# Kernel optimization log

Hardware: AMD Instinct MI355X
Metric: run time of the kernel (lower is better)

Reference implementation:

```python
import math
import jax, jax.numpy as jnp
import numpy as np

NHID = 1024
HEADS = 16
SEQ = 1024
BATCH = 8


def setup_inputs() -> dict:
    key = jax.random.key(0)
    ks = jax.random.split(key, 12)
    s = 0.02
    inp = {
        "query": jax.random.normal(ks[0], (SEQ, BATCH, NHID), jnp.float32),
        "key": jax.random.normal(ks[1], (SEQ, BATCH, NHID), jnp.float32),
        "value": jax.random.normal(ks[2], (SEQ, BATCH, NHID), jnp.float32),
        "qs_p": jax.random.normal(ks[3], (1, 1, NHID), jnp.float32) * s,
        "ks_p": jax.random.normal(ks[4], (1, 1, NHID), jnp.float32) * s,
        "vs_p": jax.random.normal(ks[5], (1, 1, NHID), jnp.float32) * s,
        "Wq": jax.random.normal(ks[6], (NHID, NHID), jnp.float32) * s,
        "bq": jax.random.normal(ks[7], (NHID,), jnp.float32) * s,
        "Wzf": jax.random.normal(ks[8], (2 * NHID, NHID), jnp.float32) * s,
        "bzf": jax.random.normal(ks[9], (2 * NHID,), jnp.float32) * s,
    }
    # additive causal mask, viewed as (1,1,S,S) and added to scores
    causal = jnp.triu(jnp.ones((SEQ, SEQ), jnp.float32), k=1) * (-1e9)
    inp["attn_mask"] = causal
    return inp


def reference(query, key, value, qs_p, ks_p, vs_p, Wq, bq, Wzf, bzf, attn_mask):
    nhid = NHID
    heads = HEADS
    dim = nhid // heads

    # sigmoid gates on Q/K/V scales
    qs = jax.nn.sigmoid(qs_p)              # (1,1,nhid)
    ks_g = jax.nn.sigmoid(ks_p)
    vs_in = jax.nn.sigmoid(vs_p)

    # QRNNLayer(window=1, output_gate=False) on single-step vs:
    # z = tanh(Wz vs + bz), f = sigmoid(Wf vs + bf), h = f * z (h0 = 0)
    zf = jnp.einsum('abn,mn->abm', vs_in, Wzf) + bzf   # (1,1,2*nhid)
    z = jnp.tanh(zf[..., :nhid])
    f = jax.nn.sigmoid(zf[..., nhid:])
    vs = f * z                                          # (1,1,nhid)

    # q projection (k,v have no Linear with defaults)
    q_lin = jnp.einsum('sbn,mn->sbm', query, Wq) + bq

    q = qs * q_lin       # (S,B,nhid)
    k = ks_g * key
    v = vs * value

    # seq-first -> batch-first, split heads
    def split_heads(t):
        t = t.transpose(1, 0, 2)                         # (B,S,nhid)
        B, S, _ = t.shape
        return t.reshape(B, S, heads, dim).transpose(0, 2, 1, 3)  # (B,H,S,d)

    qh, kh, vh = split_heads(q), split_heads(k), split_heads(v)

    scores = jnp.einsum('bhqd,bhkd->bhqk', qh, kh) / math.sqrt(dim)
    scores = scores + attn_mask[None, None]              # (B,H,S,S)
    weights = jax.nn.softmax(scores, axis=-1)
    mix = jnp.einsum('bhqk,bhkd->bhqd', weights, vh)     # (B,H,S,d)

    B = mix.shape[0]
    mix = mix.transpose(0, 2, 1, 3).reshape(B, -1, nhid)  # (B,S,nhid)
    mix = mix.transpose(1, 0, 2)                          # (S,B,nhid) seq-first
    return mix, weights
```

## Files before the change

### kernel.cpp

```cpp
#include <hip/hip_runtime.h>

typedef unsigned short u16;
typedef unsigned int   u32;
typedef float  f32x4  __attribute__((ext_vector_type(4)));
typedef short  bf16x8 __attribute__((ext_vector_type(8)));
typedef unsigned short u16x8 __attribute__((ext_vector_type(8)));
typedef unsigned short u16x4 __attribute__((ext_vector_type(4)));
typedef unsigned int   u32x2 __attribute__((ext_vector_type(2)));

#define DEV __device__ __forceinline__

constexpr int S  = 1024;
constexpr int BB = 8;
constexpr int NH = 1024;
constexpr int H  = 16;

DEV u16 f2bf(float f) {
  union { float f; unsigned u; } v{f};
  unsigned r = v.u + 0x7FFFu + ((v.u >> 16) & 1u);
  return (u16)(r >> 16);
}
DEV float sigm(float x) { return 1.0f / (1.0f + __expf(-x)); }
DEV float exp2a(float x) { float r; asm("v_exp_f32 %0, %1" : "=v"(r) : "v"(x)); return r; }

DEV void gload_lds16(const void* g, void* l) {
  __builtin_amdgcn_global_load_lds(
      (const __attribute__((address_space(1))) unsigned int*)g,
      (__attribute__((address_space(3))) unsigned int*)l, 16, 0, 0);
}

DEV f32x4 ntload4(const float* p) {
  return __builtin_nontemporal_load((const f32x4*)p);
}
DEV void ntstore4(f32x4 v, float* p) {
  __builtin_nontemporal_store(v, (f32x4*)p);
}

constexpr float SC = 0.18033688f;

__global__ __launch_bounds__(256) void k_prep(
    const float* __restrict__ query, const float* __restrict__ key,
    const float* __restrict__ value, const float* __restrict__ qs_p,
    const float* __restrict__ ks_p,  const float* __restrict__ vs_p,
    const float* __restrict__ Wq,   const float* __restrict__ bq,
    const float* __restrict__ Wzf,  const float* __restrict__ bzf,
    u16* __restrict__ qx, u16* __restrict__ kout, u16* __restrict__ vout,
    float* __restrict__ vsg, float* __restrict__ bq2, u16* __restrict__ wq_bf)
{
  __shared__ float tile[64][65];
  if (blockIdx.x >= 4096) {
    int m = (blockIdx.x - 4096) * 4 + (threadIdx.x >> 6);
    int l = threadIdx.x & 63;
    const float* wz = Wzf + (size_t)m * NH;
    const float* wf = Wzf + (size_t)(m + NH) * NH;
    int base = l * 16;
    float za = 0.f, fa = 0.f;
#pragma unroll
    for (int i = 0; i < 16; i += 4) {
      f32x4 vp  = *(const f32x4*)(vs_p + base + i);
      f32x4 wzv = *(const f32x4*)(wz + base + i);
      f32x4 wfv = *(const f32x4*)(wf + base + i);
      float v0 = sigm(vp.x), v1 = sigm(vp.y), v2 = sigm(vp.z), v3 = sigm(vp.w);
      za += v0 * wzv.x + v1 * wzv.y + v2 * wzv.z + v3 * wzv.w;
      fa += v0 * wfv.x + v1 * wfv.y + v2 * wfv.z + v3 * wfv.w;
    }
#pragma unroll
    for (int off = 1; off < 64; off <<= 1) {
      za += __shfl_xor(za, off);
      fa += __shfl_xor(fa, off);
    }
    float z   = tanhf(za + bzf[m]);
    float f   = sigm(fa + bzf[m + NH]);
    float qsm = sigm(qs_p[m]);
    if (l == 0) {
      vsg[m] = f * z;
      bq2[m] = qsm * bq[m] * SC;
    }
    float qss = qsm * SC;
    const float* wqr = Wq + (size_t)m * NH;
    u16* dst = wq_bf + (size_t)m * NH + base;
#pragma unroll
    for (int i = 0; i < 16; i += 4) {
      f32x4 wv = *(const f32x4*)(wqr + base + i);
      u16x4 o;
      o[0] = f2bf(qss * wv.x); o[1] = f2bf(qss * wv.y);
      o[2] = f2bf(qss * wv.z); o[3] = f2bf(qss * wv.w);
      *(u16x4*)(dst + i) = o;
    }
    return;
  }
  size_t idx = ((size_t)blockIdx.x * 256 + threadIdx.x) * 8;
  {
    f32x4 a = ntload4(query + idx);
    f32x4 b = ntload4(query + idx + 4);
    u16x8 o;
    o[0] = f2bf(a.x); o[1] = f2bf(a.y); o[2] = f2bf(a.z); o[3] = f2bf(a.w);
    o[4] = f2bf(b.x); o[5] = f2bf(b.y); o[6] = f2bf(b.z); o[7] = f2bf(b.w);
    *(u16x8*)(qx + idx) = o;
  }
  {
    int n0 = (int)(idx & 1023);
    int b  = (int)((idx >> 10) & 7);
    int s  = (int)(idx >> 13);
    f32x4 a  = ntload4(key + idx);
    f32x4 c  = ntload4(key + idx + 4);
    f32x4 k0 = *(const f32x4*)(ks_p + n0);
    f32x4 k1 = *(const f32x4*)(ks_p + n0 + 4);
    int h = n0 >> 6, d0 = n0 & 63;
    u16* dst = kout + (((size_t)(b * H + h) * S + s) * 64 + d0);
    u16x8 o;
    o[0] = f2bf(a.x * sigm(k0.x)); o[1] = f2bf(a.y * sigm(k0.y));
    o[2] = f2bf(a.z * sigm(k0.z)); o[3] = f2bf(a.w * sigm(k0.w));
    o[4] = f2bf(c.x * sigm(k1.x)); o[5] = f2bf(c.y * sigm(k1.y));
    o[6] = f2bf(c.z * sigm(k1.z)); o[7] = f2bf(c.w * sigm(k1.w));
    *(u16x8*)dst = o;
  }
  if (blockIdx.x < 2048) {
    int bh = blockIdx.x >> 4, kt = blockIdx.x & 15;
    int b = bh >> 4, h = bh & 15;
    int t = threadIdx.x;
    int sp = t >> 2, c0 = (t & 3) * 16;
    const float* src = value + ((size_t)(kt * 64 + sp) * (BB * NH) + b * NH + h * 64 + c0);
#pragma unroll
    for (int i = 0; i < 16; i += 4) {
      f32x4 v = ntload4(src + i);
      tile[sp][c0 + i + 0] = v.x;
      tile[sp][c0 + i + 1] = v.y;
      tile[sp][c0 + i + 2] = v.z;
      tile[sp][c0 + i + 3] = v.w;
    }
    __syncthreads();
    int d = t >> 2, s0 = (t & 3) * 16;
    u16* dst = vout + (((size_t)bh * 16 + kt) * 64 + d) * 64 + s0;
    u16x8 o0, o1;
#pragma unroll
    for (int i = 0; i < 8; ++i) o0[i] = f2bf(tile[s0 + i][d]);
#pragma unroll
    for (int i = 0; i < 8; ++i) o1[i] = f2bf(tile[s0 + 8 + i][d]);
    *(u16x8*)dst       = o0;
    *(u16x8*)(dst + 8) = o1;
  }
}

__global__ __launch_bounds__(512, 4) void k_attn(
    const u16* __restrict__ qx, const u16* __restrict__ wqb,
    const float* __restrict__ bq2, const u16* __restrict__ kws,
    const u16* __restrict__ vtw, const float* __restrict__ vsg,
    float* __restrict__ mix, float* __restrict__ wout)
{
  __shared__ __align__(16) char smem[65536];
  int bid = blockIdx.x;
  int b = bid & 7;
  int idx = bid >> 3;
  int h = idx & 15, t = 7 - (idx >> 4);
  int bh = b * 16 + h;
  int tid = threadIdx.x, w = tid >> 6, l = tid & 63;
  int g = l >> 4, lq = l & 15;
  int q0 = t * 128;
  int myq = q0 + 16 * w + lq;
  int jmax = 2 * t + 1;
  int jd = 2 * t + (w >> 2);
  float* wbase = wout + (size_t)bh * S * S;
  int srow = l >> 3, sblk = l & 7;

  u16* As = (u16*)smem;
  u16* Bs = (u16*)(smem + 32768);
  u16* Qs = (u16*)smem;
  u16* KVf = (u16*)(smem + 16384);
  u16* K2  = (u16*)smem;
  u16* V2  = (u16*)(smem + 24576);

  {
    size_t qrowbase = (size_t)(q0 * 8 + b) * 1024;
    auto stageA = [&](int kt, int buf) {
#pragma unroll
      for (int ii = 0; ii < 2; ++ii) {
        int i = w * 2 + ii;
        int row = i * 8 + srow;
        int blk = sblk ^ (row & 7);
        gload_lds16(qx + qrowbase + (size_t)row * 8192 + kt * 64 + blk * 8,
                    &As[buf * 8192 + i * 512]);
      }
    };
    auto stageB = [&](int kt, int buf) {
      int row = w * 8 + srow;
      int blk = sblk ^ (row & 7);
      gload_lds16(wqb + (size_t)(h * 64 + row) * 1024 + kt * 64 + blk * 8,
                  &Bs[buf * 4096 + w * 512]);
    };
    f32x4 acc[4];
    f32x4 zero4 = {0.f, 0.f, 0.f, 0.f};
#pragma unroll
    for (int fj = 0; fj < 4; ++fj) acc[fj] = zero4;
    stageA(0, 0); stageB(0, 0);
    for (int kt = 0; kt < 16; ++kt) {
      asm volatile("s_waitcnt vmcnt(0)" ::: "memory");
      __builtin_amdgcn_sched_barrier(0);
      __builtin_amdgcn_s_barrier();
      __builtin_amdgcn_sched_barrier(0);
      if (kt < 15) { stageA(kt + 1, (kt + 1) & 1); stageB(kt + 1, (kt + 1) & 1); }
      __builtin_amdgcn_sched_barrier(0);
      int ab = (kt & 1) * 8192, bb = (kt & 1) * 4096;
      __builtin_amdgcn_s_setprio(1);
#pragma unroll
      for (int kk = 0; kk < 2; ++kk) {
        int ar = 16 * w + lq;
        bf16x8 av = *(const bf16x8*)&As[ab + ar * 64 + ((((kk << 2) + g) ^ (ar & 7)) << 3)];
#pragma unroll
        for (int fj = 0; fj < 4; ++fj) {
          int br = fj * 16 + lq;
          bf16x8 bv = *(const bf16x8*)&Bs[bb + br * 64 + ((((kk << 2) + g) ^ (br & 7)) << 3)];
          acc[fj] = __builtin_amdgcn_mfma_f32_16x16x32_bf16(av, bv, acc[fj], 0, 0, 0);
        }
      }
      __builtin_amdgcn_s_setprio(0);
    }
    float bq4[4];
#pragma unroll
    for (int fj = 0; fj < 4; ++fj) bq4[fj] = bq2[h * 64 + fj * 16 + lq];
#pragma unroll
    for (int fj = 0; fj < 4; ++fj) {
      int d = fj * 16 + lq;
#pragma unroll
      for (int r = 0; r < 4; ++r) {
        int qrow = 16 * w + (g << 2) + r;
        Qs[qrow * 64 + (((fj * 2 + (d >> 3 & 1)) ^ (qrow & 7)) << 3) + (d & 7)] =
            f2bf(acc[fj][r] + bq4[fj]);
      }
    }
    __syncthreads();
  }
  bf16x8 qa[2];
#pragma unroll
  for (int kk = 0; kk < 2; ++kk) {
    int qr = 16 * w + lq;
    qa[kk] = *(const bf16x8*)&Qs[qr * 64 + ((((kk << 2) + g) ^ (qr & 7)) << 3)];
  }
  asm volatile("s_waitcnt lgkmcnt(0)" ::: "memory");
  __builtin_amdgcn_sched_barrier(0);
  __builtin_amdgcn_s_barrier();

  auto stageK1 = [&](int j, int buf) {
    int row = w * 8 + srow;
    int blk = sblk ^ (row & 7);
    gload_lds16(kws + ((size_t)bh * S + j * 64 + row) * 64 + blk * 8,
                &KVf[buf * 4096 + w * 512]);
  };

  stageK1(0, 0);
  if (jmax >= 1) stageK1(1, 1);
  if (jmax >= 2) stageK1(2, 2);
  float lsum = 0.f;
  for (int j = 0; j <= jmax; ++j) {
    if (j + 2 <= jmax)      asm volatile("s_waitcnt vmcnt(2)" ::: "memory");
    else if (j + 1 <= jmax) asm volatile("s_waitcnt vmcnt(1)" ::: "memory");
    else                    asm volatile("s_waitcnt vmcnt(0)" ::: "memory");
    __builtin_amdgcn_sched_barrier(0);
    __builtin_amdgcn_s_barrier();
    __builtin_amdgcn_sched_barrier(0);
    if (j + 3 <= jmax) stageK1(j + 3, (j + 3) & 3);
    __builtin_amdgcn_sched_barrier(0);
    if (j <= jd) {
      int jb = (j & 3) * 4096;
      f32x4 sacc[4];
      f32x4 zero4 = {0.f, 0.f, 0.f, 0.f};
#pragma unroll
      for (int fj = 0; fj < 4; ++fj) sacc[fj] = zero4;
      __builtin_amdgcn_s_setprio(1);
#pragma unroll
      for (int kk = 0; kk < 2; ++kk)
#pragma unroll
        for (int fj = 0; fj < 4; ++fj) {
          int kr = fj * 16 + lq;
          bf16x8 kb = *(const bf16x8*)&KVf[jb + kr * 64 + ((((kk << 2) + g) ^ (kr & 7)) << 3)];
          sacc[fj] = __builtin_amdgcn_mfma_f32_16x16x32_bf16(kb, qa[kk], sacc[fj], 0, 0, 0);
        }
      __builtin_amdgcn_s_setprio(0);
      if (j < jd) {
#pragma unroll
        for (int fj = 0; fj < 4; ++fj)
#pragma unroll
          for (int r = 0; r < 4; ++r) lsum += exp2a(sacc[fj][r]);
      } else {
#pragma unroll
        for (int fj = 0; fj < 4; ++fj)
#pragma unroll
          for (int r = 0; r < 4; ++r) {
            int ki = j * 64 + fj * 16 + 4 * g + r;
            if (ki <= myq) lsum += exp2a(sacc[fj][r]);
          }
      }
    }
  }
  lsum += __shfl_xor(lsum, 16);
  lsum += __shfl_xor(lsum, 32);
  float invl = 1.0f / lsum;

  __builtin_amdgcn_s_barrier();

  auto stageK2 = [&](int j, int buf) {
    int row = w * 8 + srow;
    int blk = sblk ^ (row & 7);
    gload_lds16(kws + ((size_t)bh * S + j * 64 + row) * 64 + blk * 8,
                smem + buf * 8192 + w * 1024);
  };
  auto stageV2 = [&](int j, int buf) {
    int row = w * 8 + srow;
    int blk = sblk ^ (row & 7);
    gload_lds16(vtw + (((size_t)bh * 16 + j) * 64 + row) * 64 + blk * 8,
                smem + 24576 + buf * 8192 + w * 1024);
  };
  stageK2(0, 0); stageV2(0, 0);
  stageK2(1, 1); stageV2(1, 1);
  int bcur = 0;
  f32x4 oacc[4];
  {
    f32x4 zero4 = {0.f, 0.f, 0.f, 0.f};
#pragma unroll
    for (int db = 0; db < 4; ++db) oacc[db] = zero4;
  }
  char* pb = smem + 49152 + w * 2048;
  int pswz = (lq & 7) * 16;
  for (int j = 0; j <= jmax; ++j) {
    if (j == 0)            asm volatile("s_waitcnt vmcnt(2)" ::: "memory");
    else if (j == 1) {
      if (jmax >= 2)       asm volatile("s_waitcnt vmcnt(6)" ::: "memory");
      else                 asm volatile("s_waitcnt vmcnt(4)" ::: "memory");
    }
    else if (j < jmax)     asm volatile("s_waitcnt vmcnt(10)" ::: "memory");
    else                   asm volatile("s_waitcnt vmcnt(8)" ::: "memory");
    __builtin_amdgcn_sched_barrier(0);
    __builtin_amdgcn_s_barrier();
    __builtin_amdgcn_sched_barrier(0);
    if (j + 2 <= jmax) {
      int tb = bcur + 2; if (tb >= 3) tb -= 3;
      stageK2(j + 2, tb); stageV2(j + 2, tb);
    }
    __builtin_amdgcn_sched_barrier(0);
    if (j > jd) {
      f32x4 z4 = {0.f, 0.f, 0.f, 0.f};
#pragma unroll
      for (int fj = 0; fj < 4; ++fj)
        ntstore4(z4, wbase + (size_t)myq * S + j * 64 + fj * 16 + g * 4);
    } else {
      int kbase = bcur * 4096;
      f32x4 sacc[4];
      f32x4 zero4 = {0.f, 0.f, 0.f, 0.f};
#pragma unroll
      for (int fj = 0; fj < 4; ++fj) sacc[fj] = zero4;
      __builtin_amdgcn_s_setprio(1);
#pragma unroll
      for (int kk = 0; kk < 2; ++kk)
#pragma unroll
        for (int fj = 0; fj < 4; ++fj) {
          int kr = fj * 16 + lq;
          bf16x8 kb = *(const bf16x8*)&K2[kbase + kr * 64 + ((((kk << 2) + g) ^ (kr & 7)) << 3)];
          sacc[fj] = __builtin_amdgcn_mfma_f32_16x16x32_bf16(kb, qa[kk], sacc[fj], 0, 0, 0);
        }
      __builtin_amdgcn_s_setprio(0);
      bool diag = (j == jd);
      float p0[4], p1[4], p2[4], p3[4];
#pragma unroll
      for (int fj = 0; fj < 4; ++fj) {
        float* pp = fj == 0 ? p0 : fj == 1 ? p1 : fj == 2 ? p2 : p3;
#pragma unroll
        for (int r = 0; r < 4; ++r) {
          float e = exp2a(sacc[fj][r]) * invl;
          if (diag) {
            int ki = j * 64 + fj * 16 + 4 * g + r;
            if (ki > myq) e = 0.f;
          }
          pp[r] = e;
        }
      }
#pragma unroll
      for (int fj = 0; fj < 4; ++fj) {
        float* pp = fj == 0 ? p0 : fj == 1 ? p1 : fj == 2 ? p2 : p3;
        u32 w0, w1;
        asm("v_cvt_pk_bf16_f32 %0, %1, %2" : "=v"(w0) : "v"(pp[0]), "v"(pp[1]));
        asm("v_cvt_pk_bf16_f32 %0, %1, %2" : "=v"(w1) : "v"(pp[2]), "v"(pp[3]));
        u32x2 wv = {w0, w1};
        *(u32x2*)(pb + lq * 128 + ((fj * 32 + g * 8) ^ pswz)) = wv;
      }
#pragma unroll
      for (int fj = 0; fj < 4; ++fj) {
        float* pp = fj == 0 ? p0 : fj == 1 ? p1 : fj == 2 ? p2 : p3;
        f32x4 f4 = {pp[0], pp[1], pp[2], pp[3]};
        ntstore4(f4, wbase + (size_t)myq * S + j * 64 + fj * 16 + g * 4);
      }
      asm volatile("s_waitcnt lgkmcnt(0)" ::: "memory");
      __builtin_amdgcn_sched_barrier(0);
      __builtin_amdgcn_s_setprio(1);
#pragma unroll
      for (int kk = 0; kk < 2; ++kk) {
        bf16x8 pa = *(const bf16x8*)(pb + lq * 128 + ((kk * 64 + g * 16) ^ pswz));
#pragma unroll
        for (int db = 0; db < 4; ++db) {
          int d = db * 16 + lq;
          bf16x8 vb = *(const bf16x8*)&V2[bcur * 4096 + d * 64 + ((((kk << 2) + g) ^ (d & 7)) << 3)];
          oacc[db] = __builtin_amdgcn_mfma_f32_16x16x32_bf16(pa, vb, oacc[db], 0, 0, 0);
        }
      }
      __builtin_amdgcn_s_setprio(0);
    }
    bcur = (bcur == 2) ? 0 : bcur + 1;
  }

  float vs4[4];
#pragma unroll
  for (int db = 0; db < 4; ++db) vs4[db] = vsg[h * 64 + db * 16 + lq];
#pragma unroll
  for (int db = 0; db < 4; ++db) {
#pragma unroll
    for (int r = 0; r < 4; ++r) {
      int qi = q0 + 16 * w + 4 * g + r;
      __builtin_nontemporal_store(oacc[db][r] * vs4[db],
          mix + (size_t)(qi * BB + b) * NH + h * 64 + db * 16 + lq);
    }
  }

  {
    f32x4 z4 = {0.f, 0.f, 0.f, 0.f};
    int cstart = (jmax + 1) * 64;
    for (int lr = 0; lr < 16; ++lr) {
      float* rowp = wbase + (size_t)(q0 + 16 * w + lr) * S;
      for (int c = cstart + l * 4; c < S; c += 256)
        ntstore4(z4, rowp + c);
    }
  }
}

extern "C" void kernel_launch(void* const* d_in, const int* in_sizes, int n_in,
                              void* d_out, int out_size, void* d_ws, size_t ws_size,
                              hipStream_t stream) {
  (void)in_sizes; (void)n_in; (void)out_size; (void)ws_size;
  const float* query = (const float*)d_in[0];
  const float* key   = (const float*)d_in[1];
  const float* value = (const float*)d_in[2];
  const float* qs_p  = (const float*)d_in[3];
  const float* ks_p  = (const float*)d_in[4];
  const float* vs_p  = (const float*)d_in[5];
  const float* Wq    = (const float*)d_in[6];
  const float* bq    = (const float*)d_in[7];
  const float* Wzf   = (const float*)d_in[8];
  const float* bzf   = (const float*)d_in[9];

  char* ws = (char*)d_ws;
  float* vsg  = (float*)(ws + 0x1000);
  float* bq2  = (float*)(ws + 0x2000);
  u16* wq_bf  = (u16*)(ws + 0x4000);
  u16* qx_bf  = (u16*)(ws + 0x204000);
  u16* k_ws   = (u16*)(ws + 0x1204000);
  u16* vt_ws  = (u16*)(ws + 0x2204000);

  float* mix  = (float*)d_out;
  float* wout = mix + (size_t)S * BB * NH;

  k_prep<<<4352, 256, 0, stream>>>(query, key, value, qs_p, ks_p, vs_p,
                                   Wq, bq, Wzf, bzf,
                                   qx_bf, k_ws, vt_ws, vsg, bq2, wq_bf);
  k_attn<<<1024, 512, 0, stream>>>(qx_bf, wq_bf, bq2, k_ws, vt_ws, vsg,
                                   mix, wout);
}
```

Baseline: 224.1 us.

## Halve attention query tile to 64 rows with 256-thread blocks

```diff
diff --git a/kernel.cpp b/kernel.cpp
--- a/kernel.cpp
+++ b/kernel.cpp
@@ -142,51 +142,51 @@
   }
 }
 
-__global__ __launch_bounds__(512, 4) void k_attn(
+__global__ __launch_bounds__(256, 4) void k_attn(
     const u16* __restrict__ qx, const u16* __restrict__ wqb,
     const float* __restrict__ bq2, const u16* __restrict__ kws,
     const u16* __restrict__ vtw, const float* __restrict__ vsg,
     float* __restrict__ mix, float* __restrict__ wout)
 {
-  __shared__ __align__(16) char smem[65536];
+  __shared__ __align__(16) char smem[40960];
   int bid = blockIdx.x;
   int b = bid & 7;
   int idx = bid >> 3;
-  int h = idx & 15, t = 7 - (idx >> 4);
+  int h = idx & 15, t = 15 - (idx >> 4);
   int bh = b * 16 + h;
   int tid = threadIdx.x, w = tid >> 6, l = tid & 63;
   int g = l >> 4, lq = l & 15;
-  int q0 = t * 128;
+  int q0 = t * 64;
   int myq = q0 + 16 * w + lq;
-  int jmax = 2 * t + 1;
-  int jd = 2 * t + (w >> 2);
+  int jmax = t;
   float* wbase = wout + (size_t)bh * S * S;
   int srow = l >> 3, sblk = l & 7;
 
   u16* As = (u16*)smem;
-  u16* Bs = (u16*)(smem + 32768);
+  u16* Bs = (u16*)(smem + 16384);
   u16* Qs = (u16*)smem;
-  u16* KVf = (u16*)(smem + 16384);
-  u16* K2  = (u16*)smem;
-  u16* V2  = (u16*)(smem + 24576);
+  u16* K1 = (u16*)(smem + 8192);
+  u16* K2 = (u16*)(smem + 8192);
+  u16* V2 = (u16*)(smem + 24576);
 
   {
-    size_t qrowbase = (size_t)(q0 * 8 + b) * 1024;
     auto stageA = [&](int kt, int buf) {
 #pragma unroll
       for (int ii = 0; ii < 2; ++ii) {
-        int i = w * 2 + ii;
-        int row = i * 8 + srow;
+        int row = w * 16 + ii * 8 + srow;
         int blk = sblk ^ (row & 7);
-        gload_lds16(qx + qrowbase + (size_t)row * 8192 + kt * 64 + blk * 8,
-                    &As[buf * 8192 + i * 512]);
+        gload_lds16(qx + ((size_t)((q0 + row) * 8 + b) * 1024 + kt * 64 + blk * 8),
+                    &As[buf * 4096 + (w * 2 + ii) * 512]);
       }
     };
     auto stageB = [&](int kt, int buf) {
-      int row = w * 8 + srow;
-      int blk = sblk ^ (row & 7);
-      gload_lds16(wqb + (size_t)(h * 64 + row) * 1024 + kt * 64 + blk * 8,
-                  &Bs[buf * 4096 + w * 512]);
+#pragma unroll
+      for (int ii = 0; ii < 2; ++ii) {
+        int row = w * 16 + ii * 8 + srow;
+        int blk = sblk ^ (row & 7);
+        gload_lds16(wqb + ((size_t)(h * 64 + row) * 1024 + kt * 64 + blk * 8),
+                    &Bs[buf * 4096 + (w * 2 + ii) * 512]);
+      }
     };
     f32x4 acc[4];
     f32x4 zero4 = {0.f, 0.f, 0.f, 0.f};
@@ -200,7 +200,7 @@
       __builtin_amdgcn_sched_barrier(0);
       if (kt < 15) { stageA(kt + 1, (kt + 1) & 1); stageB(kt + 1, (kt + 1) & 1); }
       __builtin_amdgcn_sched_barrier(0);
-      int ab = (kt & 1) * 8192, bb = (kt & 1) * 4096;
+      int ab = (kt & 1) * 4096, bb = (kt & 1) * 4096;
       __builtin_amdgcn_s_setprio(1);
 #pragma unroll
       for (int kk = 0; kk < 2; ++kk) {
@@ -241,55 +241,55 @@
   __builtin_amdgcn_s_barrier();
 
   auto stageK1 = [&](int j, int buf) {
-    int row = w * 8 + srow;
-    int blk = sblk ^ (row & 7);
-    gload_lds16(kws + ((size_t)bh * S + j * 64 + row) * 64 + blk * 8,
-                &KVf[buf * 4096 + w * 512]);
+#pragma unroll
+    for (int ii = 0; ii < 2; ++ii) {
+      int row = w * 16 + ii * 8 + srow;
+      int blk = sblk ^ (row & 7);
+      gload_lds16(kws + ((size_t)bh * S + j * 64 + row) * 64 + blk * 8,
+                  &K1[buf * 4096 + (w * 2 + ii) * 512]);
+    }
   };
 
   stageK1(0, 0);
   if (jmax >= 1) stageK1(1, 1);
-  if (jmax >= 2) stageK1(2, 2);
   float lsum = 0.f;
   for (int j = 0; j <= jmax; ++j) {
-    if (j + 2 <= jmax)      asm volatile("s_waitcnt vmcnt(2)" ::: "memory");
-    else if (j + 1 <= jmax) asm volatile("s_waitcnt vmcnt(1)" ::: "memory");
-    else                    asm volatile("s_waitcnt vmcnt(0)" ::: "memory");
+    if (j + 1 <= jmax) asm volatile("s_waitcnt vmcnt(2)" ::: "memory");
+    else               asm volatile("s_waitcnt vmcnt(0)" ::: "memory");
     __builtin_amdgcn_sched_barrier(0);
     __builtin_amdgcn_s_barrier();
     __builtin_amdgcn_sched_barrier(0);
-    if (j + 3 <= jmax) stageK1(j + 3, (j + 3) & 3);
-    __builtin_amdgcn_sched_barrier(0);
-    if (j <= jd) {
-      int jb = (j & 3) * 4096;
-      f32x4 sacc[4];
-      f32x4 zero4 = {0.f, 0.f, 0.f, 0.f};
-#pragma unroll
-      for (int fj = 0; fj < 4; ++fj) sacc[fj] = zero4;
-      __builtin_amdgcn_s_setprio(1);
-#pragma unroll
-      for (int kk = 0; kk < 2; ++kk)
-#pragma unroll
-        for (int fj = 0; fj < 4; ++fj) {
-          int kr = fj * 16 + lq;
-          bf16x8 kb = *(const bf16x8*)&KVf[jb + kr * 64 + ((((kk << 2) + g) ^ (kr & 7)) << 3)];
-          sacc[fj] = __builtin_amdgcn_mfma_f32_16x16x32_bf16(kb, qa[kk], sacc[fj], 0, 0, 0);
+    if (j + 2 <= jmax) { int tb = j + 2; while (tb >= 3) tb -= 3; stageK1(j + 2, tb); }
+    __builtin_amdgcn_sched_barrier(0);
+    int jb = j; while (jb >= 3) jb -= 3;
+    jb *= 4096;
+    f32x4 sacc[4];
+    f32x4 zero4 = {0.f, 0.f, 0.f, 0.f};
+#pragma unroll
+    for (int fj = 0; fj < 4; ++fj) sacc[fj] = zero4;
+    __builtin_amdgcn_s_setprio(1);
+#pragma unroll
+    for (int kk = 0; kk < 2; ++kk)
+#pragma unroll
+      for (int fj = 0; fj < 4; ++fj) {
+        int kr = fj * 16 + lq;
+        bf16x8 kb = *(const bf16x8*)&K1[jb + kr * 64 + ((((kk << 2) + g) ^ (kr & 7)) << 3)];
+        sacc[fj] = __builtin_amdgcn_mfma_f32_16x16x32_bf16(kb, qa[kk], sacc[fj], 0, 0, 0);
+      }
+    __builtin_amdgcn_s_setprio(0);
+    if (j < jmax) {
+#pragma unroll
+      for (int fj = 0; fj < 4; ++fj)
+#pragma unroll
+        for (int r = 0; r < 4; ++r) lsum += exp2a(sacc[fj][r]);
+    } else {
+#pragma unroll
+      for (int fj = 0; fj < 4; ++fj)
+#pragma unroll
+        for (int r = 0; r < 4; ++r) {
+          int ki = j * 64 + fj * 16 + 4 * g + r;
+          if (ki <= myq) lsum += exp2a(sacc[fj][r]);
         }
-      __builtin_amdgcn_s_setprio(0);
-      if (j < jd) {
-#pragma unroll
-        for (int fj = 0; fj < 4; ++fj)
-#pragma unroll
-          for (int r = 0; r < 4; ++r) lsum += exp2a(sacc[fj][r]);
-      } else {
-#pragma unroll
-        for (int fj = 0; fj < 4; ++fj)
-#pragma unroll
-          for (int r = 0; r < 4; ++r) {
-            int ki = j * 64 + fj * 16 + 4 * g + r;
-            if (ki <= myq) lsum += exp2a(sacc[fj][r]);
-          }
-      }
     }
   }
   lsum += __shfl_xor(lsum, 16);
@@ -299,111 +299,99 @@
   __builtin_amdgcn_s_barrier();
 
   auto stageK2 = [&](int j, int buf) {
-    int row = w * 8 + srow;
-    int blk = sblk ^ (row & 7);
-    gload_lds16(kws + ((size_t)bh * S + j * 64 + row) * 64 + blk * 8,
-                smem + buf * 8192 + w * 1024);
+#pragma unroll
+    for (int ii = 0; ii < 2; ++ii) {
+      int row = w * 16 + ii * 8 + srow;
+      int blk = sblk ^ (row & 7);
+      gload_lds16(kws + ((size_t)bh * S + j * 64 + row) * 64 + blk * 8,
+                  &K2[buf * 4096 + (w * 2 + ii) * 512]);
+    }
   };
   auto stageV2 = [&](int j, int buf) {
-    int row = w * 8 + srow;
-    int blk = sblk ^ (row & 7);
-    gload_lds16(vtw + (((size_t)bh * 16 + j) * 64 + row) * 64 + blk * 8,
-                smem + 24576 + buf * 8192 + w * 1024);
+#pragma unroll
+    for (int ii = 0; ii < 2; ++ii) {
+      int row = w * 16 + ii * 8 + srow;
+      int blk = sblk ^ (row & 7);
+      gload_lds16(vtw + (((size_t)bh * 16 + j) * 64 + row) * 64 + blk * 8,
+                  &V2[buf * 4096 + (w * 2 + ii) * 512]);
+    }
   };
   stageK2(0, 0); stageV2(0, 0);
-  stageK2(1, 1); stageV2(1, 1);
-  int bcur = 0;
   f32x4 oacc[4];
   {
     f32x4 zero4 = {0.f, 0.f, 0.f, 0.f};
 #pragma unroll
     for (int db = 0; db < 4; ++db) oacc[db] = zero4;
   }
-  char* pb = smem + 49152 + w * 2048;
+  char* pb = smem + w * 2048;
   int pswz = (lq & 7) * 16;
   for (int j = 0; j <= jmax; ++j) {
-    if (j == 0)            asm volatile("s_waitcnt vmcnt(2)" ::: "memory");
-    else if (j == 1) {
-      if (jmax >= 2)       asm volatile("s_waitcnt vmcnt(6)" ::: "memory");
-      else                 asm volatile("s_waitcnt vmcnt(4)" ::: "memory");
-    }
-    else if (j < jmax)     asm volatile("s_waitcnt vmcnt(10)" ::: "memory");
-    else                   asm volatile("s_waitcnt vmcnt(8)" ::: "memory");
+    if (j == 0) asm volatile("s_waitcnt vmcnt(0)" ::: "memory");
+    else        asm volatile("s_waitcnt vmcnt(4)" ::: "memory");
     __builtin_amdgcn_sched_barrier(0);
     __builtin_amdgcn_s_barrier();
     __builtin_amdgcn_sched_barrier(0);
-    if (j + 2 <= jmax) {
-      int tb = bcur + 2; if (tb >= 3) tb -= 3;
-      stageK2(j + 2, tb); stageV2(j + 2, tb);
-    }
-    __builtin_amdgcn_sched_barrier(0);
-    if (j > jd) {
-      f32x4 z4 = {0.f, 0.f, 0.f, 0.f};
-#pragma unroll
-      for (int fj = 0; fj < 4; ++fj)
-        ntstore4(z4, wbase + (size_t)myq * S + j * 64 + fj * 16 + g * 4);
-    } else {
-      int kbase = bcur * 4096;
-      f32x4 sacc[4];
-      f32x4 zero4 = {0.f, 0.f, 0.f, 0.f};
-#pragma unroll
-      for (int fj = 0; fj < 4; ++fj) sacc[fj] = zero4;
-      __builtin_amdgcn_s_setprio(1);
-#pragma unroll
-      for (int kk = 0; kk < 2; ++kk)
-#pragma unroll
-        for (int fj = 0; fj < 4; ++fj) {
-          int kr = fj * 16 + lq;
-          bf16x8 kb = *(const bf16x8*)&K2[kbase + kr * 64 + ((((kk << 2) + g) ^ (kr & 7)) << 3)];
-          sacc[fj] = __builtin_amdgcn_mfma_f32_16x16x32_bf16(kb, qa[kk], sacc[fj], 0, 0, 0);
+    if (j < jmax) { stageK2(j + 1, (j + 1) & 1); stageV2(j + 1, (j + 1) & 1); }
+    __builtin_amdgcn_sched_barrier(0);
+    int kbase = (j & 1) * 4096;
+    f32x4 sacc[4];
+    f32x4 zero4 = {0.f, 0.f, 0.f, 0.f};
+#pragma unroll
+    for (int fj = 0; fj < 4; ++fj) sacc[fj] = zero4;
+    __builtin_amdgcn_s_setprio(1);
+#pragma unroll
+    for (int kk = 0; kk < 2; ++kk)
+#pragma unroll
+      for (int fj = 0; fj < 4; ++fj) {
+        int kr = fj * 16 + lq;
+        bf16x8 kb = *(const bf16x8*)&K2[kbase + kr * 64 + ((((kk << 2) + g) ^ (kr & 7)) << 3)];
+        sacc[fj] = __builtin_amdgcn_mfma_f32_16x16x32_bf16(kb, qa[kk], sacc[fj], 0, 0, 0);
+      }
+    __builtin_amdgcn_s_setprio(0);
+    bool diag = (j == jmax);
+    float p0[4], p1[4], p2[4], p3[4];
+#pragma unroll
+    for (int fj = 0; fj < 4; ++fj) {
+      float* pp = fj == 0 ? p0 : fj == 1 ? p1 : fj == 2 ? p2 : p3;
+#pragma unroll
+      for (int r = 0; r < 4; ++r) {
+        float e = exp2a(sacc[fj][r]) * invl;
+        if (diag) {
+          int ki = j * 64 + fj * 16 + 4 * g + r;
+          if (ki > myq) e = 0.f;
         }
-      __builtin_amdgcn_s_setprio(0);
-      bool diag = (j == jd);
-      float p0[4], p1[4], p2[4], p3[4];
-#pragma unroll
-      for (int fj = 0; fj < 4; ++fj) {
-        float* pp = fj == 0 ? p0 : fj == 1 ? p1 : fj == 2 ? p2 : p3;
-#pragma unroll
-        for (int r = 0; r < 4; ++r) {
-          float e = exp2a(sacc[fj][r]) * invl;
-          if (diag) {
-            int ki = j * 64 + fj * 16 + 4 * g + r;
-            if (ki > myq) e = 0.f;
-          }
-          pp[r] = e;
-        }
-      }
-#pragma unroll
-      for (int fj = 0; fj < 4; ++fj) {
-        float* pp = fj == 0 ? p0 : fj == 1 ? p1 : fj == 2 ? p2 : p3;
-        u32 w0, w1;
-        asm("v_cvt_pk_bf16_f32 %0, %1, %2" : "=v"(w0) : "v"(pp[0]), "v"(pp[1]));
-        asm("v_cvt_pk_bf16_f32 %0, %1, %2" : "=v"(w1) : "v"(pp[2]), "v"(pp[3]));
-        u32x2 wv = {w0, w1};
-        *(u32x2*)(pb + lq * 128 + ((fj * 32 + g * 8) ^ pswz)) = wv;
-      }
-#pragma unroll
-      for (int fj = 0; fj < 4; ++fj) {
-        float* pp = fj == 0 ? p0 : fj == 1 ? p1 : fj == 2 ? p2 : p3;
-        f32x4 f4 = {pp[0], pp[1], pp[2], pp[3]};
-        ntstore4(f4, wbase + (size_t)myq * S + j * 64 + fj * 16 + g * 4);
-      }
-      asm volatile("s_waitcnt lgkmcnt(0)" ::: "memory");
-      __builtin_amdgcn_sched_barrier(0);
-      __builtin_amdgcn_s_setprio(1);
-#pragma unroll
-      for (int kk = 0; kk < 2; ++kk) {
-        bf16x8 pa = *(const bf16x8*)(pb + lq * 128 + ((kk * 64 + g * 16) ^ pswz));
-#pragma unroll
-        for (int db = 0; db < 4; ++db) {
-          int d = db * 16 + lq;
-          bf16x8 vb = *(const bf16x8*)&V2[bcur * 4096 + d * 64 + ((((kk << 2) + g) ^ (d & 7)) << 3)];
-          oacc[db] = __builtin_amdgcn_mfma_f32_16x16x32_bf16(pa, vb, oacc[db], 0, 0, 0);
-        }
-      }
-      __builtin_amdgcn_s_setprio(0);
-    }
-    bcur = (bcur == 2) ? 0 : bcur + 1;
+        pp[r] = e;
+      }
+    }
+#pragma unroll
+    for (int fj = 0; fj < 4; ++fj) {
+      float* pp = fj == 0 ? p0 : fj == 1 ? p1 : fj == 2 ? p2 : p3;
+      u32 w0, w1;
+      asm("v_cvt_pk_bf16_f32 %0, %1, %2" : "=v"(w0) : "v"(pp[0]), "v"(pp[1]));
+      asm("v_cvt_pk_bf16_f32 %0, %1, %2" : "=v"(w1) : "v"(pp[2]), "v"(pp[3]));
+      u32x2 wv = {w0, w1};
+      *(u32x2*)(pb + lq * 128 + ((fj * 32 + g * 8) ^ pswz)) = wv;
+    }
+#pragma unroll
+    for (int fj = 0; fj < 4; ++fj) {
+      float* pp = fj == 0 ? p0 : fj == 1 ? p1 : fj == 2 ? p2 : p3;
+      f32x4 f4 = {pp[0], pp[1], pp[2], pp[3]};
+      *(f32x4*)(wbase + (size_t)myq * S + j * 64 + fj * 16 + g * 4) = f4;
+    }
+    asm volatile("s_waitcnt lgkmcnt(0)" ::: "memory");
+    __builtin_amdgcn_sched_barrier(0);
+    __builtin_amdgcn_s_setprio(1);
+#pragma unroll
+    for (int kk = 0; kk < 2; ++kk) {
+      bf16x8 pa = *(const bf16x8*)(pb + lq * 128 + ((kk * 64 + g * 16) ^ pswz));
+#pragma unroll
+      for (int db = 0; db < 4; ++db) {
+        int d = db * 16 + lq;
+        bf16x8 vb = *(const bf16x8*)&V2[(j & 1) * 4096 + d * 64 + ((((kk << 2) + g) ^ (d & 7)) << 3)];
+        oacc[db] = __builtin_amdgcn_mfma_f32_16x16x32_bf16(pa, vb, oacc[db], 0, 0, 0);
+      }
+    }
+    __builtin_amdgcn_s_setprio(0);
   }
 
   float vs4[4];
@@ -414,8 +402,7 @@
 #pragma unroll
     for (int r = 0; r < 4; ++r) {
       int qi = q0 + 16 * w + 4 * g + r;
-      __builtin_nontemporal_store(oacc[db][r] * vs4[db],
-          mix + (size_t)(qi * BB + b) * NH + h * 64 + db * 16 + lq);
+      mix[(size_t)(qi * BB + b) * NH + h * 64 + db * 16 + lq] = oacc[db][r] * vs4[db];
     }
   }
 
@@ -459,6 +446,6 @@
   k_prep<<<4352, 256, 0, stream>>>(query, key, value, qs_p, ks_p, vs_p,
                                    Wq, bq, Wzf, bzf,
                                    qx_bf, k_ws, vt_ws, vsg, bq2, wq_bf);
-  k_attn<<<1024, 512, 0, stream>>>(qx_bf, wq_bf, bq2, k_ws, vt_ws, vsg,
+  k_attn<<<2048, 256, 0, stream>>>(qx_bf, wq_bf, bq2, k_ws, vt_ws, vsg,
                                    mix, wout);
 }
```

After: 187.3 us. 1.2x faster.
